# Kernel tuning notes

Hardware: AMD Instinct MI355X
Metric: run time of the kernel (lower is better)

Reference implementation:

```python
import jax, jax.numpy as jnp
import numpy as np

WS = 8            # window size (square)
HEADS = 16
HEAD_DIM = 32
DIM = 512
NEG_INF = float('-inf')


def _create_mask(ws, disp, upper_lower, left_right):
    size = ws * ws
    m = np.zeros((size, size), dtype=np.float32)
    d = disp
    if upper_lower:
        m[-d * ws:, :-d * ws] = NEG_INF
        m[:-d * ws, -d * ws:] = NEG_INF
    if left_right:
        m = m.reshape(ws, ws, ws, ws)
        m[:, -d:, :, :-d] = NEG_INF
        m[:, :-d, :, -d:] = NEG_INF
        m = m.reshape(size, size)
    return m


def _relative_indices(ws):
    coords = np.array([[x, y] for x in range(ws) for y in range(ws)])  # [ws^2, 2]
    dist = coords[None, :, :] - coords[:, None, :]                      # [ws^2, ws^2, 2]
    dist += ws - 1
    return dist.astype(np.int64)


_REL_IDX = _relative_indices(WS)                      # [64, 64, 2]
_UL_MASK = jnp.asarray(_create_mask(WS, WS // 2, True, False))   # [64, 64]
_LR_MASK = jnp.asarray(_create_mask(WS, WS // 2, False, True))   # [64, 64]


def setup_inputs() -> dict:
    key = jax.random.key(0)
    ks = jax.random.split(key, 5)
    b, n = 16, 64
    return {
        'x': jax.random.normal(ks[0], (b, n, n, DIM), dtype=jnp.float32),
        'w_qkv': jax.random.normal(ks[1], (3 * HEADS * HEAD_DIM, DIM), dtype=jnp.float32) * 0.02,
        'pos_embedding': jax.random.normal(ks[2], (2 * WS - 1, 2 * WS - 1), dtype=jnp.float32),
        'w_out': jax.random.normal(ks[3], (DIM, HEADS * HEAD_DIM), dtype=jnp.float32) * 0.02,
        'b_out': jax.random.normal(ks[4], (DIM,), dtype=jnp.float32) * 0.02,
    }


def reference(x, w_qkv, pos_embedding, w_out, b_out):
    disp = WS // 2
    scale = HEAD_DIM ** -0.5
    b, n_h, n_w, _ = x.shape
    nw_h, nw_w = n_h // WS, n_w // WS

    # cyclic shift (shifted=True)
    x = jnp.roll(x, shift=(-disp, -disp), axis=(1, 2))

    qkv = x @ w_qkv.T                                   # [b, n_h, n_w, 3*h*d]
    qkv = qkv.reshape(b, nw_h, WS, nw_w, WS, 3, HEADS, HEAD_DIM)
    # -> [3, b, heads, n_windows, window_tokens, head_dim]
    qkv = qkv.transpose(5, 0, 6, 1, 3, 2, 4, 7).reshape(
        3, b, HEADS, nw_h * nw_w, WS * WS, HEAD_DIM)
    q, k, v = qkv[0], qkv[1], qkv[2]

    dots = jnp.einsum('bhwid,bhwjd->bhwij', q, k) * scale
    # relative position bias
    dots = dots + pos_embedding[_REL_IDX[:, :, 0], _REL_IDX[:, :, 1]]
    # shift masks: last window-row and last window-column
    dots = dots.at[:, :, -nw_w:].add(_UL_MASK)
    dots = dots.at[:, :, nw_w - 1::nw_w].add(_LR_MASK)

    attn = jax.nn.softmax(dots, axis=-1)
    out = jnp.einsum('bhwij,bhwjd->bhwid', attn, v)     # [b,h,nw,ws^2,d]

    out = out.reshape(b, HEADS, nw_h, nw_w, WS, WS, HEAD_DIM)
    out = out.transpose(0, 2, 4, 3, 5, 1, 6).reshape(b, n_h, n_w, HEADS * HEAD_DIM)
    out = out @ w_out.T + b_out

    out = jnp.roll(out, shift=(disp, disp), axis=(1, 2))
    return out
```

## Files before the change

### kernel.cpp

```cpp
#include <hip/hip_runtime.h>
#include <hip/hip_bf16.h>
#include <stdint.h>

typedef __bf16 bf16;
typedef __attribute__((ext_vector_type(4))) float f32x4;
typedef __attribute__((ext_vector_type(8))) bf16 bf16x8;
typedef __attribute__((ext_vector_type(4))) bf16 bf16x4;

#define AS1 __attribute__((address_space(1)))
#define AS3 __attribute__((address_space(3)))

static __device__ __forceinline__ void gload_lds16(const bf16* g, bf16* l) {
  __builtin_amdgcn_global_load_lds((const AS1 void*)g, (AS3 void*)l, 16, 0, 0);
}

#define BAR __builtin_amdgcn_s_barrier()
#define SCHED0 __builtin_amdgcn_sched_barrier(0)
#define VMC_(n) asm volatile("s_waitcnt vmcnt(" #n ")" ::: "memory")
#define VMC(n) VMC_(n)
#define LGKM0 asm volatile("s_waitcnt lgkmcnt(0)" ::: "memory")

#define STAGE_A(gsrc, dst, kt_) do {                                          \
  _Pragma("unroll") for (int s_ = 0; s_ < 4; ++s_) {                          \
    int idx_ = s_ * 256 + tid;                                                \
    int r_ = idx_ >> 3, c_ = idx_ & 7;                                        \
    gload_lds16((gsrc) + (size_t)r_ * 512 + ((kt_) << 6) + ((c_ ^ (r_ & 7)) << 3), \
                (dst) + idx_ * 8);                                            \
  }                                                                           \
} while (0)

#define LOADB(ktq, NCOLX) do {                                                \
  const bf16* bp_ = Bptr + (size_t)(ktq) * ((size_t)(NCOLX) * 64);            \
  _Pragma("unroll") for (int cb_ = 0; cb_ < 4; ++cb_)                         \
  _Pragma("unroll") for (int ks_ = 0; ks_ < 2; ++ks_)                         \
    bfr[cb_][ks_] = *(const bf16x8*)(bp_ + cb_ * 128 + (size_t)ks_ * (NCOLX) * 32); \
} while (0)

#define KLOOP_BD(Ag, NCOLX)                                                   \
  f32x4 acc[4][4] = {};                                                       \
  bf16x8 af[4][2], bfr[4][2];                                                 \
  STAGE_A(Ag, SA0, 0);                                                        \
  LOADB(0, NCOLX);                                                            \
  VMC(8); BAR;                                                                \
  STAGE_A(Ag, SA1, 1);                                                        \
  _Pragma("unroll 2")                                                         \
  for (int kt = 0; kt < 8; ++kt) {                                            \
    bf16* Ap = (kt & 1) ? SA1 : SA0;                                          \
    _Pragma("unroll") for (int i_ = 0; i_ < 4; ++i_) {                        \
      int ra_ = wr + i_ * 16 + lr;                                            \
      _Pragma("unroll") for (int ks_ = 0; ks_ < 2; ++ks_)                     \
        af[i_][ks_] = *(const bf16x8*)(Ap + ra_ * 64 + (((ks_ * 4 + lg) ^ (ra_ & 7)) << 3)); \
    }                                                                         \
    LGKM0; SCHED0;                                                            \
    __builtin_amdgcn_s_setprio(1);                                            \
    _Pragma("unroll") for (int i_ = 0; i_ < 4; ++i_)                          \
    _Pragma("unroll") for (int j_ = 0; j_ < 4; ++j_)                          \
    _Pragma("unroll") for (int ks_ = 0; ks_ < 2; ++ks_)                       \
      acc[i_][j_] = __builtin_amdgcn_mfma_f32_16x16x32_bf16(                  \
          af[i_][ks_], bfr[j_][ks_], acc[i_][j_], 0, 0, 0);                   \
    __builtin_amdgcn_s_setprio(0);                                            \
    if (kt < 7) LOADB(kt + 1, NCOLX);                                         \
    if (kt < 7) { VMC(8); }                                                   \
    BAR;                                                                      \
    if (kt < 6) STAGE_A(Ag, Ap, kt + 2);                                      \
  }

__global__ __launch_bounds__(256) void prep_x(const float* __restrict__ x,
                                              bf16* __restrict__ xst) {
  int m = blockIdx.x * 256 + threadIdx.x;
  int b = m >> 12, win = (m >> 6) & 63, t = m & 63;
  int ip = ((win >> 3) << 3) + (t >> 3);
  int jp = ((win & 7) << 3) + (t & 7);
  int io = (ip + 4) & 63, jo = (jp + 4) & 63;
  const float* src = x + ((((size_t)(b << 6) + io) << 6) + jo) * 512;
  bf16* dst = xst + (size_t)m * 8;
  #pragma unroll 4
  for (int kb = 0; kb < 64; ++kb) {
    float4 v0 = *(const float4*)(src + kb * 8);
    float4 v1 = *(const float4*)(src + kb * 8 + 4);
    bf16x8 o = { (bf16)v0.x, (bf16)v0.y, (bf16)v0.z, (bf16)v0.w,
                 (bf16)v1.x, (bf16)v1.y, (bf16)v1.z, (bf16)v1.w };
    *(bf16x8*)(dst + (size_t)kb * 524288) = o;
  }
}

__global__ __launch_bounds__(256) void prep_w(const float* __restrict__ wqkv,
                                              const float* __restrict__ wout,
                                              bf16* __restrict__ wqkv_bt,
                                              bf16* __restrict__ wout_bt) {
  int r = blockIdx.x * 8 + (threadIdx.x >> 5);
  int lane = threadIdx.x & 31;
  const float* src;
  bf16* dstb;
  int ncol, col;
  float sc = 1.0f;
  if (r < 1536) {
    int part = r >> 9, h = (r >> 5) & 15, d = r & 31;
    src = wqkv + (size_t)r * 512; dstb = wqkv_bt; ncol = 1536;
    col = h * 96 + part * 32 + d;
    if (part == 0) sc = 0.17677669529663689f;
  } else {
    src = wout + (size_t)(r - 1536) * 512; dstb = wout_bt; ncol = 512; col = r - 1536;
  }
  #pragma unroll
  for (int kb = lane; kb < 64; kb += 32) {
    float4 v0 = *(const float4*)(src + kb * 8);
    float4 v1 = *(const float4*)(src + kb * 8 + 4);
    bf16x8 o = { (bf16)(v0.x * sc), (bf16)(v0.y * sc), (bf16)(v0.z * sc), (bf16)(v0.w * sc),
                 (bf16)(v1.x * sc), (bf16)(v1.y * sc), (bf16)(v1.z * sc), (bf16)(v1.w * sc) };
    *(bf16x8*)(dstb + ((size_t)kb * ncol + col) * 8) = o;
  }
}

__global__ __launch_bounds__(256) void prep_bias(const float* __restrict__ pos,
                                                 float* __restrict__ bias4) {
  for (int idx = threadIdx.x; idx < 4 * 4096; idx += 256) {
    int ty = idx >> 12, ij = idx & 4095;
    int i = ij >> 6, j = ij & 63;
    int rx = ((j >> 3) - (i >> 3)) + 7;
    int ry = ((j & 7) - (i & 7)) + 7;
    float v = pos[rx * 15 + ry];
    if ((ty & 1) && (((i ^ j) >> 5) & 1)) v = -1e30f;
    if ((ty & 2) && (((i ^ j) >> 2) & 1)) v = -1e30f;
    bias4[idx] = v;
  }
}

#define LOADAF(dst, ktq) do {                                                 \
  _Pragma("unroll") for (int i_ = 0; i_ < 2; ++i_)                            \
  _Pragma("unroll") for (int ks_ = 0; ks_ < 2; ++ks_)                         \
    dst[i_][ks_] = *(const bf16x8*)(Aptr + ((size_t)((ktq) * 8 + ks_ * 4 + lg)) * 524288 + i_ * 128); \
} while (0)

#define LOADB_H(set, ktq, hf) do {                                            \
  const bf16* bp_ = Bptr + (size_t)(ktq) * 98304 + (hf) * 384;                \
  _Pragma("unroll") for (int cb_ = 0; cb_ < 3; ++cb_)                         \
  _Pragma("unroll") for (int ks_ = 0; ks_ < 2; ++ks_)                         \
    set[cb_][ks_] = *(const bf16x8*)(bp_ + cb_ * 128 + ks_ * 49152);          \
} while (0)

#define MM3(afs, bs, j0)                                                      \
  _Pragma("unroll") for (int i_ = 0; i_ < 2; ++i_)                            \
  _Pragma("unroll") for (int jj_ = 0; jj_ < 3; ++jj_)                         \
  _Pragma("unroll") for (int ks_ = 0; ks_ < 2; ++ks_)                         \
    acc[i_][(j0) + jj_] = __builtin_amdgcn_mfma_f32_16x16x32_bf16(            \
        afs[i_][ks_], bs[jj_][ks_], acc[i_][(j0) + jj_], 0, 0, 0);

#define KTS(CUR, NXT, KT_, V2) do {                                           \
  VMC(6); SCHED0;                                                             \
  __builtin_amdgcn_s_setprio(1); MM3(CUR, bfrX, 0);                           \
  __builtin_amdgcn_s_setprio(0);                                              \
  if ((KT_) < 7) { LOADAF(NXT, (KT_) + 1); LOADB_H(bfrX, (KT_) + 1, 0); }     \
  VMC(V2); SCHED0;                                                            \
  __builtin_amdgcn_s_setprio(1); MM3(CUR, bfrY, 3);                           \
  __builtin_amdgcn_s_setprio(0);                                              \
  if ((KT_) < 7) LOADB_H(bfrY, (KT_) + 1, 1);                                 \
} while (0)

__global__ __launch_bounds__(256, 3) void qkv_attn(
    const bf16* __restrict__ xst, const bf16* __restrict__ wb2,
    const float* __restrict__ bias4, bf16* __restrict__ ao) {
  __shared__ bf16 smb[12288];

  const int tid = threadIdx.x, wave = tid >> 6, lane = tid & 63;
  const int ww = wave >> 1, rh = wave & 1;
  const int lr = lane & 15, lg = lane >> 4;

  int bid = blockIdx.x;
  bid = (bid & 7) * 1024 + (bid >> 3);
  const int mt = bid >> 4, h = bid & 15;

  const bf16* Aptr = xst + ((size_t)(mt * 128 + ww * 64 + rh * 32 + lr)) * 8;
  const bf16* Bptr = wb2 + (((size_t)lg * 1536) + h * 96 + lr) * 8;

  f32x4 acc[2][6] = {};
  bf16x8 afA[2][2], afB[2][2], bfrX[3][2], bfrY[3][2];

  LOADAF(afA, 0); LOADB_H(bfrX, 0, 0); LOADB_H(bfrY, 0, 1);
  KTS(afA, afB, 0, 10);
  KTS(afB, afA, 1, 10);
  KTS(afA, afB, 2, 10);
  KTS(afB, afA, 3, 10);
  KTS(afA, afB, 4, 10);
  KTS(afB, afA, 5, 10);
  KTS(afA, afB, 6, 10);
  KTS(afB, afA, 7, 0);

  bf16* Eu = smb + ww * 6144;
  bf16* Ev = Eu + 4096;
  #pragma unroll
  for (int i = 0; i < 2; ++i)
    #pragma unroll
    for (int r = 0; r < 4; ++r) {
      int row = rh * 32 + i * 16 + (lg << 2) + r;
      #pragma unroll
      for (int j = 0; j < 4; ++j) {
        int c = j * 16 + lr;
        Eu[row * 64 + (c ^ ((row & 7) << 3))] = (bf16)acc[i][j][r];
      }
      #pragma unroll
      for (int j = 4; j < 6; ++j) {
        int cv = (j - 4) * 16 + lr;
        Ev[cv * 64 + (row ^ ((cv & 7) << 3))] = (bf16)acc[i][j][r];
      }
    }
  LGKM0; BAR;

  bf16x8 qf[2], kf[4];
  #pragma unroll
  for (int i = 0; i < 2; ++i) {
    int ra = rh * 32 + i * 16 + lr;
    qf[i] = *(const bf16x8*)(Eu + ra * 64 + ((lg << 3) ^ ((ra & 7) << 3)));
  }
  #pragma unroll
  for (int j = 0; j < 4; ++j) {
    int rb = j * 16 + lr;
    kf[j] = *(const bf16x8*)(Eu + rb * 64 + ((32 + (lg << 3)) ^ ((rb & 7) << 3)));
  }
  f32x4 s[2][4] = {};
  #pragma unroll
  for (int i = 0; i < 2; ++i)
    #pragma unroll
    for (int j = 0; j < 4; ++j)
      s[i][j] = __builtin_amdgcn_mfma_f32_16x16x32_bf16(qf[i], kf[j], s[i][j], 0, 0, 0);

  const int gw = mt * 2 + ww;
  const int win = gw & 63;
  const int ty = ((win >= 56) ? 1 : 0) | (((win & 7) == 7) ? 2 : 0);
  const float* bt = bias4 + ty * 4096;
  #pragma unroll
  for (int i = 0; i < 2; ++i)
    #pragma unroll
    for (int r = 0; r < 4; ++r) {
      int grow = rh * 32 + i * 16 + (lg << 2) + r;
      #pragma unroll
      for (int j = 0; j < 4; ++j)
        s[i][j][r] += bt[grow * 64 + j * 16 + lr];
    }
  #pragma unroll
  for (int i = 0; i < 2; ++i)
    #pragma unroll
    for (int r = 0; r < 4; ++r) {
      float mx = fmaxf(fmaxf(s[i][0][r], s[i][1][r]), fmaxf(s[i][2][r], s[i][3][r]));
      mx = fmaxf(mx, __shfl_xor(mx, 1));
      mx = fmaxf(mx, __shfl_xor(mx, 2));
      mx = fmaxf(mx, __shfl_xor(mx, 4));
      mx = fmaxf(mx, __shfl_xor(mx, 8));
      float sum = 0.f;
      #pragma unroll
      for (int j = 0; j < 4; ++j) { s[i][j][r] = __expf(s[i][j][r] - mx); sum += s[i][j][r]; }
      sum += __shfl_xor(sum, 1);
      sum += __shfl_xor(sum, 2);
      sum += __shfl_xor(sum, 4);
      sum += __shfl_xor(sum, 8);
      float inv = 1.0f / sum;
      #pragma unroll
      for (int j = 0; j < 4; ++j) s[i][j][r] *= inv;
    }
  BAR;
  #pragma unroll
  for (int i = 0; i < 2; ++i)
    #pragma unroll
    for (int r = 0; r < 4; ++r) {
      int row = rh * 32 + i * 16 + (lg << 2) + r;
      #pragma unroll
      for (int j = 0; j < 4; ++j) {
        int c = j * 16 + lr;
        Eu[row * 64 + (c ^ ((row & 7) << 3))] = (bf16)s[i][j][r];
      }
    }
  LGKM0; SCHED0;
  bf16x8 vf[2][2];
  #pragma unroll
  for (int kk = 0; kk < 2; ++kk)
    #pragma unroll
    for (int nj = 0; nj < 2; ++nj) {
      int dv = nj * 16 + lr;
      vf[kk][nj] = *(const bf16x8*)(Ev + dv * 64 + ((kk * 32 + (lg << 3)) ^ ((dv & 7) << 3)));
    }
  f32x4 o[2][2] = {};
  #pragma unroll
  for (int kk = 0; kk < 2; ++kk)
    #pragma unroll
    for (int mi = 0; mi < 2; ++mi) {
      int ra = rh * 32 + mi * 16 + lr;
      bf16x8 pa = *(const bf16x8*)(Eu + ra * 64 + ((kk * 32 + (lg << 3)) ^ ((ra & 7) << 3)));
      #pragma unroll
      for (int nj = 0; nj < 2; ++nj)
        o[mi][nj] = __builtin_amdgcn_mfma_f32_16x16x32_bf16(pa, vf[kk][nj], o[mi][nj], 0, 0, 0);
    }
  bf16* dst = ao + ((size_t)(mt * 128 + ww * 64)) * 512 + h * 32;
  #pragma unroll
  for (int mi = 0; mi < 2; ++mi)
    #pragma unroll
    for (int r = 0; r < 4; ++r) {
      int t = rh * 32 + mi * 16 + (lg << 2) + r;
      #pragma unroll
      for (int nj = 0; nj < 2; ++nj)
        dst[(size_t)t * 512 + nj * 16 + lr] = (bf16)o[mi][nj][r];
    }
}

__global__ __launch_bounds__(256, 3) void gemm_out(
    const bf16* __restrict__ ao, const bf16* __restrict__ wob,
    const float* __restrict__ bout, float* __restrict__ out) {
  __shared__ bf16 SA[2][8192];
  bf16* SA0 = SA[0]; bf16* SA1 = SA[1];

  const int tid = threadIdx.x, wave = tid >> 6, lane = tid & 63;
  int bid = blockIdx.x;
  bid = (bid & 7) * 256 + (bid >> 3);
  const int mt = bid >> 2, nt = bid & 3;
  const bf16* Ag = ao + ((size_t)mt * 128) * 512;
  const int wr = (wave >> 1) << 6, wc = (wave & 1) << 6;
  const int lr = lane & 15, lg = lane >> 4;
  const bf16* Bptr = wob + (((size_t)lg * 512) + nt * 128 + wc + lr) * 8;

  KLOOP_BD(Ag, 512)

  float bv[4];
  #pragma unroll
  for (int j = 0; j < 4; ++j) bv[j] = bout[nt * 128 + wc + j * 16 + lr];
  #pragma unroll
  for (int i = 0; i < 4; ++i)
    #pragma unroll
    for (int r = 0; r < 4; ++r) {
      int m = (mt << 7) + wr + i * 16 + (lg << 2) + r;
      int b = m >> 12, win = (m >> 6) & 63, t = m & 63;
      int ip = ((win >> 3) << 3) + (t >> 3);
      int jp = ((win & 7) << 3) + (t & 7);
      int io = (ip + 4) & 63, jo = (jp + 4) & 63;
      float* orow = out + ((((size_t)(b << 6) + io) << 6) + jo) * 512 + nt * 128 + wc;
      #pragma unroll
      for (int j = 0; j < 4; ++j)
        orow[j * 16 + lr] = acc[i][j][r] + bv[j];
    }
}

extern "C" void kernel_launch(void* const* d_in, const int* in_sizes, int n_in,
                              void* d_out, int out_size, void* d_ws, size_t ws_size,
                              hipStream_t stream) {
  const float* x    = (const float*)d_in[0];
  const float* wqkv = (const float*)d_in[1];
  const float* pos  = (const float*)d_in[2];
  const float* wout = (const float*)d_in[3];
  const float* bout = (const float*)d_in[4];
  float* out = (float*)d_out;

  char* ws = (char*)d_ws;
  bf16* xst     = (bf16*)(ws);
  bf16* ao      = (bf16*)(ws + 67108864);
  bf16* wqkv_bt = (bf16*)(ws + 268435456);
  bf16* wout_bt = (bf16*)(ws + 270008320);
  float* bias4  = (float*)(ws + 270532608);

  prep_x<<<dim3(256), dim3(256), 0, stream>>>(x, xst);
  prep_w<<<dim3(256), dim3(256), 0, stream>>>(wqkv, wout, wqkv_bt, wout_bt);
  prep_bias<<<dim3(1), dim3(256), 0, stream>>>(pos, bias4);
  qkv_attn<<<dim3(8192), dim3(256), 0, stream>>>(xst, wqkv_bt, bias4, ao);
  gemm_out<<<dim3(2048), dim3(256), 0, stream>>>(ao, wout_bt, bout, out);
}
```

Baseline: 264.1 us.

## Deepen qkv_attn register prefetch to two stages and widen prep_x grid

The QKV GEMM main loop now keeps two k-steps of A and B fragments in flight in registers instead of one, issuing loads two iterations ahead and adjusting the vmcnt waits to match. This hides more global-load latency but raises register pressure, so the occupancy hint drops from 3 to 2 blocks per CU. Separately, prep_x splits each token's 64 k-blocks across the 4 waves of a block and launches 4x more blocks, giving the memory-bound conversion more parallelism.

```diff
diff --git a/kernel.cpp b/kernel.cpp
--- a/kernel.cpp
+++ b/kernel.cpp
@@ -67,7 +67,8 @@
 
 __global__ __launch_bounds__(256) void prep_x(const float* __restrict__ x,
                                               bf16* __restrict__ xst) {
-  int m = blockIdx.x * 256 + threadIdx.x;
+  int m = blockIdx.x * 64 + (threadIdx.x & 63);
+  int w = threadIdx.x >> 6;
   int b = m >> 12, win = (m >> 6) & 63, t = m & 63;
   int ip = ((win >> 3) << 3) + (t >> 3);
   int jp = ((win & 7) << 3) + (t & 7);
@@ -75,7 +76,8 @@
   const float* src = x + ((((size_t)(b << 6) + io) << 6) + jo) * 512;
   bf16* dst = xst + (size_t)m * 8;
   #pragma unroll 4
-  for (int kb = 0; kb < 64; ++kb) {
+  for (int it = 0; it < 16; ++it) {
+    int kb = w * 16 + it;
     float4 v0 = *(const float4*)(src + kb * 8);
     float4 v1 = *(const float4*)(src + kb * 8 + 4);
     bf16x8 o = { (bf16)v0.x, (bf16)v0.y, (bf16)v0.z, (bf16)v0.w,
@@ -146,18 +148,21 @@
     acc[i_][(j0) + jj_] = __builtin_amdgcn_mfma_f32_16x16x32_bf16(            \
         afs[i_][ks_], bs[jj_][ks_], acc[i_][(j0) + jj_], 0, 0, 0);
 
-#define KTS(CUR, NXT, KT_, V2) do {                                           \
-  VMC(6); SCHED0;                                                             \
-  __builtin_amdgcn_s_setprio(1); MM3(CUR, bfrX, 0);                           \
+#define KTS2(CUR, KT_, V1, V2, ISS) do {                                      \
+  VMC(V1); SCHED0;                                                            \
+  __builtin_amdgcn_s_setprio(1); MM3(CUR, bfX[(KT_) & 1], 0);                 \
   __builtin_amdgcn_s_setprio(0);                                              \
-  if ((KT_) < 7) { LOADAF(NXT, (KT_) + 1); LOADB_H(bfrX, (KT_) + 1, 0); }     \
   VMC(V2); SCHED0;                                                            \
-  __builtin_amdgcn_s_setprio(1); MM3(CUR, bfrY, 3);                           \
+  __builtin_amdgcn_s_setprio(1); MM3(CUR, bfY[(KT_) & 1], 3);                 \
   __builtin_amdgcn_s_setprio(0);                                              \
-  if ((KT_) < 7) LOADB_H(bfrY, (KT_) + 1, 1);                                 \
-} while (0)
-
-__global__ __launch_bounds__(256, 3) void qkv_attn(
+  if (ISS) {                                                                  \
+    LOADAF(CUR, (KT_) + 2);                                                   \
+    LOADB_H(bfX[(KT_) & 1], (KT_) + 2, 0);                                    \
+    LOADB_H(bfY[(KT_) & 1], (KT_) + 2, 1);                                    \
+  }                                                                           \
+} while (0)
+
+__global__ __launch_bounds__(256, 2) void qkv_attn(
     const bf16* __restrict__ xst, const bf16* __restrict__ wb2,
     const float* __restrict__ bias4, bf16* __restrict__ ao) {
   __shared__ bf16 smb[12288];
@@ -174,17 +179,19 @@
   const bf16* Bptr = wb2 + (((size_t)lg * 1536) + h * 96 + lr) * 8;
 
   f32x4 acc[2][6] = {};
-  bf16x8 afA[2][2], afB[2][2], bfrX[3][2], bfrY[3][2];
-
-  LOADAF(afA, 0); LOADB_H(bfrX, 0, 0); LOADB_H(bfrY, 0, 1);
-  KTS(afA, afB, 0, 10);
-  KTS(afB, afA, 1, 10);
-  KTS(afA, afB, 2, 10);
-  KTS(afB, afA, 3, 10);
-  KTS(afA, afB, 4, 10);
-  KTS(afB, afA, 5, 10);
-  KTS(afA, afB, 6, 10);
-  KTS(afB, afA, 7, 0);
+  bf16x8 afA[2][2], afB[2][2], bfX[2][3][2], bfY[2][3][2];
+
+  LOADAF(afA, 0); LOADB_H(bfX[0], 0, 0); LOADB_H(bfY[0], 0, 1);
+  LOADAF(afB, 1); LOADB_H(bfX[1], 1, 0); LOADB_H(bfY[1], 1, 1);
+
+  KTS2(afA, 0, 22, 16, 1);
+  KTS2(afB, 1, 22, 16, 1);
+  KTS2(afA, 2, 22, 16, 1);
+  KTS2(afB, 3, 22, 16, 1);
+  KTS2(afA, 4, 22, 16, 1);
+  KTS2(afB, 5, 22, 16, 1);
+  KTS2(afA, 6, 22, 16, 0);
+  KTS2(afB, 7, 6, 0, 0);
 
   bf16* Eu = smb + ww * 6144;
   bf16* Ev = Eu + 4096;
@@ -354,7 +361,7 @@
   bf16* wout_bt = (bf16*)(ws + 270008320);
   float* bias4  = (float*)(ws + 270532608);
 
-  prep_x<<<dim3(256), dim3(256), 0, stream>>>(x, xst);
+  prep_x<<<dim3(1024), dim3(256), 0, stream>>>(x, xst);
   prep_w<<<dim3(256), dim3(256), 0, stream>>>(wqkv, wout, wqkv_bt, wout_bt);
   prep_bias<<<dim3(1), dim3(256), 0, stream>>>(pos, bias4);
   qkv_attn<<<dim3(8192), dim3(256), 0, stream>>>(xst, wqkv_bt, bias4, ao);
```

Result: slower. 276.5 us (+4.7%).
